# Kernel optimization log

Hardware: AMD Instinct MI355X
Metric: run time of the kernel (lower is better)

The kernel has to match this reference:

```python
import jax, jax.numpy as jnp
import numpy as np
import math

D = 512; H = 8; NL = 6; VOCAB = 256; NC = 10; L = 1024; B = 4
DK = D // H
SCALE = math.sqrt(DK)
EMB_SCALE = math.sqrt(D)
EPS = 1e-5


def _pos_encoding(seq_len, d_model):
    pos = jnp.arange(seq_len, dtype=jnp.float32)[:, None]
    div = jnp.exp(-jnp.arange(0, d_model, 2, dtype=jnp.float32) / d_model * math.log(10000.0))
    pe = jnp.zeros((seq_len, d_model), dtype=jnp.float32)
    pe = pe.at[:, 0::2].set(jnp.sin(pos * div))
    pe = pe.at[:, 1::2].set(jnp.cos(pos * div))
    return pe


def _layer_norm(x, g, b):
    m = jnp.mean(x, axis=-1, keepdims=True)
    v = jnp.mean(jnp.square(x - m), axis=-1, keepdims=True)
    return (x - m) * jax.lax.rsqrt(v + EPS) * g + b


def setup_inputs() -> dict:
    key = jax.random.key(0)
    ks = jax.random.split(key, 18)
    s = 0.02  # keep activations in a sane range so softmax is not saturated
    return {
        "tokens": jax.random.randint(ks[0], (B, L), 0, VOCAB, dtype=jnp.int32),
        "emb_table": jax.random.normal(ks[1], (VOCAB, D), jnp.float32) * s,
        "Wq": jax.random.normal(ks[2], (NL, D, D), jnp.float32) * s,
        "bq": jax.random.normal(ks[3], (NL, D), jnp.float32) * s,
        "Wkv": jax.random.normal(ks[4], (NL, 2 * D, D), jnp.float32) * s,
        "bkv": jax.random.normal(ks[5], (NL, 2 * D), jnp.float32) * s,
        "Wo": jax.random.normal(ks[6], (NL, D, D), jnp.float32) * s,
        "bo": jax.random.normal(ks[7], (NL, D), jnp.float32) * s,
        "ln1_g": jnp.ones((NL, D), jnp.float32),
        "ln1_b": jnp.zeros((NL, D), jnp.float32),
        "W1": jax.random.normal(ks[8], (NL, 4 * D, D), jnp.float32) * s,
        "b1": jax.random.normal(ks[9], (NL, 4 * D), jnp.float32) * s,
        "W2": jax.random.normal(ks[10], (NL, D, 4 * D), jnp.float32) * s,
        "b2": jax.random.normal(ks[11], (NL, D), jnp.float32) * s,
        "ln2_g": jnp.ones((NL, D), jnp.float32),
        "ln2_b": jnp.zeros((NL, D), jnp.float32),
        "Wc": jax.random.normal(ks[12], (NC, D), jnp.float32) * s,
        "bc": jax.random.normal(ks[13], (NC,), jnp.float32) * s,
    }


def reference(tokens, emb_table, Wq, bq, Wkv, bkv, Wo, bo, ln1_g, ln1_b,
              W1, b1, W2, b2, ln2_g, ln2_b, Wc, bc):
    seq_len = tokens.shape[1]
    pe = _pos_encoding(seq_len, D)  # [L, D]
    x = emb_table[tokens] * EMB_SCALE + pe[None]  # [B, L, D]  (dropout = identity in eval)

    def block(x, p):
        wq, bq_, wkv, bkv_, wo, bo_, g1, be1, w1, bb1, w2, bb2, g2, be2 = p
        h = _layer_norm(x, g1, be1)
        q = h @ wq.T + bq_                       # [B, L, D]
        kv = h @ wkv.T + bkv_                    # [B, L, 2D]
        k, v = kv[..., :D], kv[..., D:]
        # split heads: [B, H, L, dk]
        q = q.reshape(*q.shape[:2], H, DK).transpose(0, 2, 1, 3)
        k = k.reshape(*k.shape[:2], H, DK).transpose(0, 2, 1, 3)
        v = v.reshape(*v.shape[:2], H, DK).transpose(0, 2, 1, 3)
        score = jnp.einsum('bhqd,bhkd->bhqk', q, k) / SCALE  # [B, H, L, L]
        attn = jax.nn.softmax(score, axis=-1)
        av = jnp.einsum('bhqk,bhkd->bhqd', attn, v)
        av = av.transpose(0, 2, 1, 3).reshape(*x.shape)      # merge heads
        x = x + (av @ wo.T + bo_)
        h2 = _layer_norm(x, g2, be2)
        ffn = jax.nn.relu(h2 @ w1.T + bb1) @ w2.T + bb2
        x = x + ffn
        return x, None

    params = (Wq, bq, Wkv, bkv, Wo, bo, ln1_g, ln1_b, W1, b1, W2, b2, ln2_g, ln2_b)
    x, _ = jax.lax.scan(block, x, params)
    return x @ Wc.T + bc  # [B, L, NC]
```

## Files before the change

### kernel.cpp

```cpp
#include <hip/hip_runtime.h>
#include <math.h>

#define D 512
#define HEADS 8
#define NLAYER 6
#define LSEQ 1024
#define BATCH 4
#define DKH 64
#define MTOK (BATCH*LSEQ)
#define EPS 1e-5f
#define EMB_SCALE 22.627416997969522f
#define INV_SCALE 0.125f

typedef __attribute__((ext_vector_type(8))) __bf16 bf16x8;
typedef __attribute__((ext_vector_type(4))) float f32x4;

__device__ __forceinline__ unsigned short f2bf(float x) {
    union { float f; unsigned u; } v; v.f = x;
    unsigned r = (v.u + 0x7FFFu + ((v.u >> 16) & 1u)) >> 16;
    return (unsigned short)r;
}
__device__ __forceinline__ unsigned pack2(float a, float b) {
    return (unsigned)f2bf(a) | ((unsigned)f2bf(b) << 16);
}
__device__ __forceinline__ void gl_lds16(const unsigned short* g, unsigned short* l) {
    __builtin_amdgcn_global_load_lds(
        (const __attribute__((address_space(1))) unsigned*)g,
        (__attribute__((address_space(3))) unsigned*)l, 16, 0, 0);
}
__device__ __forceinline__ void gload16(bf16x8& d, const unsigned short* p) {
    asm volatile("global_load_dwordx4 %0, %1, off" : "=v"(d) : "v"(p));
}

__global__ __launch_bounds__(256) void prep_kernel(
    const int* __restrict__ tokens, const float* __restrict__ emb,
    const float* __restrict__ Wq, const float* __restrict__ Wkv,
    const float* __restrict__ Wo, const float* __restrict__ W1,
    const float* __restrict__ W2, const float* __restrict__ bq,
    const float* __restrict__ bkv, unsigned short* __restrict__ wl,
    float* __restrict__ wbias, float* __restrict__ x)
{
    const int bid = blockIdx.x;
    if (bid < 9216) {
        const int l = bid / 1536;
        const int e = (bid - l * 1536) * 2048 + threadIdx.x * 8;
        const float* src;
        if      (e < 262144)  src = Wq  + (size_t)l * 262144  + e;
        else if (e < 786432)  src = Wkv + (size_t)l * 524288  + (e - 262144);
        else if (e < 1048576) src = Wo  + (size_t)l * 262144  + (e - 786432);
        else if (e < 2097152) src = W1  + (size_t)l * 1048576 + (e - 1048576);
        else                  src = W2  + (size_t)l * 1048576 + (e - 2097152);
        float4 a = *(const float4*)src;
        float4 b = *(const float4*)(src + 4);
        uint4 o;
        o.x = pack2(a.x, a.y); o.y = pack2(a.z, a.w);
        o.z = pack2(b.x, b.y); o.w = pack2(b.z, b.w);
        *(uint4*)(wl + (size_t)l * 3145728 + e) = o;
    } else if (bid == 9216) {
        for (int i = threadIdx.x; i < 9216; i += 256) {
            int l = i / 1536, j = i - l * 1536;
            wbias[i] = (j < 512) ? bq[l * 512 + j] : bkv[l * 1024 + (j - 512)];
        }
    } else {
        int row = (bid - 9217) * 2 + (threadIdx.x >> 7);
        int pos = row & (LSEQ - 1);
        int tok = tokens[row];
        int c = (threadIdx.x & 127) * 4;
        float4 e = *(const float4*)(emb + (size_t)tok * D + c);
        float o[4] = {e.x, e.y, e.z, e.w};
#pragma unroll
        for (int i = 0; i < 4; ++i) {
            int col = c + i;
            int ii = col & ~1;
            float dv = expf(-(float)ii * (9.210340371976184f / (float)D));
            float a = (float)pos * dv;
            float pe = (col & 1) ? cosf(a) : sinf(a);
            o[i] = o[i] * EMB_SCALE + pe;
        }
        float4 r; r.x = o[0]; r.y = o[1]; r.z = o[2]; r.w = o[3];
        *(float4*)(x + (size_t)row * D + c) = r;
    }
}

__global__ __launch_bounds__(256) void ln_kernel(
    const float* __restrict__ x, const float* __restrict__ g,
    const float* __restrict__ b, unsigned short* __restrict__ h)
{
    int lane = threadIdx.x & 63;
    int row = blockIdx.x * 4 + (threadIdx.x >> 6);
    const float* xr = x + (size_t)row * D + lane * 8;
    float4 v0 = *(const float4*)(xr);
    float4 v1 = *(const float4*)(xr + 4);
    float s = v0.x + v0.y + v0.z + v0.w + v1.x + v1.y + v1.z + v1.w;
#pragma unroll
    for (int off = 32; off; off >>= 1) s += __shfl_xor(s, off, 64);
    float m = s * (1.0f / D);
    float d0 = v0.x - m, d1 = v0.y - m, d2 = v0.z - m, d3 = v0.w - m;
    float d4 = v1.x - m, d5 = v1.y - m, d6 = v1.z - m, d7 = v1.w - m;
    float ss = d0*d0 + d1*d1 + d2*d2 + d3*d3 + d4*d4 + d5*d5 + d6*d6 + d7*d7;
#pragma unroll
    for (int off = 32; off; off >>= 1) ss += __shfl_xor(ss, off, 64);
    float inv = rsqrtf(ss * (1.0f / D) + EPS);
    const float* gp = g + lane * 8;
    const float* bp = b + lane * 8;
    float4 g0 = *(const float4*)(gp), g1 = *(const float4*)(gp + 4);
    float4 b0 = *(const float4*)(bp), b1 = *(const float4*)(bp + 4);
    uint4 o;
    o.x = pack2(d0 * inv * g0.x + b0.x, d1 * inv * g0.y + b0.y);
    o.y = pack2(d2 * inv * g0.z + b0.z, d3 * inv * g0.w + b0.w);
    o.z = pack2(d4 * inv * g1.x + b1.x, d5 * inv * g1.y + b1.y);
    o.w = pack2(d6 * inv * g1.z + b1.z, d7 * inv * g1.w + b1.w);
    *(uint4*)(h + (size_t)row * D + lane * 8) = o;
}

template<int OMODE, int BM, int BN, int BK>
__global__ __launch_bounds__(256) void gemm_bf16(
    const unsigned short* __restrict__ A, const unsigned short* __restrict__ W,
    const float* __restrict__ bias, const float* __restrict__ X,
    void* __restrict__ C, void* __restrict__ C2, void* __restrict__ C3,
    int M, int N, int K)
{
    constexpr int WM = BM / 64;
    constexpr int WN = 4 / WM;
    constexpr int NI = BN / (WN * 16);
    constexpr int CPB = BK / 8;
    constexpr int RPP = 2048 / BK;
    __shared__ __align__(16) unsigned short As[2][BM * BK];
    __shared__ __align__(16) unsigned short Bs[2][BN * BK];
    const int tid = threadIdx.x;
    const int wave = tid >> 6, lane = tid & 63;
    const int quad = lane >> 4, l16 = lane & 15;
    const int wm = wave / WN, wn = wave % WN;
    const int bm = blockIdx.y * BM, bn = blockIdx.x * BN;

    const int rS  = tid / CPB;
    const int ch  = tid % CPB;
    const int csw = ((ch ^ (rS & 7)) << 3);
    const unsigned short* Asrc = A + (size_t)(bm + rS) * K + csw;
    const unsigned short* Bsrc = W + (size_t)(bn + rS) * K + csw;

    f32x4 acc[4][NI];
#pragma unroll
    for (int mi = 0; mi < 4; ++mi)
#pragma unroll
        for (int ni = 0; ni < NI; ++ni) acc[mi][ni] = (f32x4){0.f, 0.f, 0.f, 0.f};

    const int nt = K / BK;

#pragma unroll
    for (int i = 0; i < BM / RPP; ++i)
        gl_lds16(Asrc + (size_t)(i * RPP) * K, &As[0][i * 2048 + tid * 8]);
#pragma unroll
    for (int i = 0; i < BN / RPP; ++i)
        gl_lds16(Bsrc + (size_t)(i * RPP) * K, &Bs[0][i * 2048 + tid * 8]);
    __syncthreads();

    for (int t = 0; t < nt; ++t) {
        const int cur = t & 1;
        if (t + 1 < nt) {
            const int k0 = (t + 1) * BK;
#pragma unroll
            for (int i = 0; i < BM / RPP; ++i)
                gl_lds16(Asrc + (size_t)(i * RPP) * K + k0, &As[cur ^ 1][i * 2048 + tid * 8]);
#pragma unroll
            for (int i = 0; i < BN / RPP; ++i)
                gl_lds16(Bsrc + (size_t)(i * RPP) * K + k0, &Bs[cur ^ 1][i * 2048 + tid * 8]);
        }
#pragma unroll
        for (int kc = 0; kc < BK / 32; ++kc) {
            const int gch = (kc << 2) | quad;
            bf16x8 af[4], bfr[NI];
#pragma unroll
            for (int mi = 0; mi < 4; ++mi) {
                const int ra = wm * 64 + mi * 16 + l16;
                af[mi] = *(const bf16x8*)&As[cur][ra * BK + ((gch ^ (ra & 7)) << 3)];
            }
#pragma unroll
            for (int ni = 0; ni < NI; ++ni) {
                const int rb = wn * (BN / WN) + ni * 16 + l16;
                bfr[ni] = *(const bf16x8*)&Bs[cur][rb * BK + ((gch ^ (rb & 7)) << 3)];
            }
#pragma unroll
            for (int mi = 0; mi < 4; ++mi)
#pragma unroll
                for (int ni = 0; ni < NI; ++ni)
                    acc[mi][ni] = __builtin_amdgcn_mfma_f32_16x16x32_bf16(
                        af[mi], bfr[ni], acc[mi][ni], 0, 0, 0);
        }
        __syncthreads();
    }

    const int er = bm + wm * 64;
    const int ec = bn + wn * (BN / WN);

    if (OMODE == 0) {
        float* Cf = (float*)C;
#pragma unroll
        for (int ni = 0; ni < NI; ++ni) {
            int c = ec + ni * 16 + l16;
            float bv = bias[c];
#pragma unroll
            for (int mi = 0; mi < 4; ++mi)
#pragma unroll
                for (int r = 0; r < 4; ++r) {
                    int m = er + mi * 16 + quad * 4 + r;
                    Cf[(size_t)m * N + c] = acc[mi][ni][r] + bv + X[(size_t)m * N + c];
                }
        }
    } else if (OMODE == 1) {
        unsigned short* Cb = (unsigned short*)C;
#pragma unroll
        for (int ni = 0; ni < NI; ++ni) {
            int c = ec + ni * 16 + l16;
            float bv = bias[c];
#pragma unroll
            for (int mi = 0; mi < 4; ++mi)
#pragma unroll
                for (int r = 0; r < 4; ++r) {
                    int m = er + mi * 16 + quad * 4 + r;
                    Cb[(size_t)m * N + c] = f2bf(fmaxf(acc[mi][ni][r] + bv, 0.f));
                }
        }
    } else {
        if (bn < 512) {
            unsigned short* Qp = (unsigned short*)C;
#pragma unroll
            for (int ni = 0; ni < NI; ++ni) {
                int c = ec + ni * 16 + l16;
                float bv = bias[c];
                int hh = c >> 6, dd = c & 63;
                size_t cbase = (size_t)(dd >> 5) * 512 + (size_t)((dd >> 3) & 3) * 128 + (dd & 7);
#pragma unroll
                for (int mi = 0; mi < 4; ++mi)
#pragma unroll
                    for (int r = 0; r < 4; ++r) {
                        int m = er + mi * 16 + quad * 4 + r;
                        int b = m >> 10, t = m & 1023;
                        Qp[(size_t)(b * 8 + hh) * 65536 + (size_t)(t >> 4) * 1024
                           + cbase + (size_t)(t & 15) * 8] =
                            f2bf((acc[mi][ni][r] + bv) * INV_SCALE);
                    }
            }
        } else if (bn < 1024) {
            unsigned short* Kp = (unsigned short*)C2;
#pragma unroll
            for (int ni = 0; ni < NI; ++ni) {
                int c = ec + ni * 16 + l16;
                float bv = bias[c];
                int c2 = c - 512;
                int hh = c2 >> 6, dd = c2 & 63;
                size_t cbase = (size_t)(dd >> 5) * 512 + (size_t)((dd >> 3) & 3) * 128 + (dd & 7);
#pragma unroll
                for (int mi = 0; mi < 4; ++mi)
#pragma unroll
                    for (int r = 0; r < 4; ++r) {
                        int m = er + mi * 16 + quad * 4 + r;
                        int b = m >> 10, t = m & 1023;
                        Kp[(size_t)(b * 8 + hh) * 65536 + (size_t)(t >> 4) * 1024
                           + cbase + (size_t)(t & 15) * 8] =
                            f2bf(acc[mi][ni][r] + bv);
                    }
            }
        } else {
            unsigned short* Vp = (unsigned short*)C3;
#pragma unroll
            for (int ni = 0; ni < NI; ++ni) {
                int c = ec + ni * 16 + l16;
                float bv = bias[c];
                int c2 = c - 1024;
                int hh = c2 >> 6, dd = c2 & 63;
                size_t dbase = (size_t)(dd >> 4) * 16384 + (size_t)(dd & 15) * 8;
#pragma unroll
                for (int mi = 0; mi < 4; ++mi) {
                    int t0 = er + mi * 16 + quad * 4;
                    int b = t0 >> 10, tt = t0 & 1023;
                    ushort4 o;
                    o.x = f2bf(acc[mi][ni][0] + bv);
                    o.y = f2bf(acc[mi][ni][1] + bv);
                    o.z = f2bf(acc[mi][ni][2] + bv);
                    o.w = f2bf(acc[mi][ni][3] + bv);
                    *(ushort4*)(Vp + (size_t)(b * 8 + hh) * 65536 + dbase
                                + (size_t)(tt >> 5) * 512
                                + (size_t)((tt >> 3) & 3) * 128 + (tt & 7)) = o;
                }
            }
        }
    }
}

__global__ __launch_bounds__(256, 1) void attn_mfma(
    const unsigned short* __restrict__ Qb, const unsigned short* __restrict__ Kb,
    const unsigned short* __restrict__ Vt, unsigned short* __restrict__ av)
{
    __shared__ float Ol[4][32][68];
    __shared__ float Ls[4][32];
    const int tid = threadIdx.x;
    const int wave = tid >> 6, lane = tid & 63;
    const int quad = lane >> 4, l16 = lane & 15;
    const int bh = blockIdx.x & 31;
    const int b = bh >> 3, h = bh & 7;
    const int q0 = (blockIdx.x >> 5) * 32;

    const unsigned short* qp = Qb + (size_t)bh * 65536 + (size_t)(q0 >> 4) * 1024 + lane * 8;
    const unsigned short* kbase = Kb + (size_t)bh * 65536 + lane * 8;
    const unsigned short* vbase = Vt + (size_t)bh * 65536 + lane * 8;

    const int sA  = ((((2 * quad) & 3) << 4) + l16) << 2;
    const int sB2 = ((((2 * quad + 1) & 3) << 4) + l16) << 2;

    f32x4 o[2][4];
#pragma unroll
    for (int qs = 0; qs < 2; ++qs)
#pragma unroll
        for (int nf = 0; nf < 4; ++nf) o[qs][nf] = (f32x4){0.f, 0.f, 0.f, 0.f};
    float lp[2] = {0.f, 0.f};

    const int j0 = wave * 256;

    bf16x8 qf[2][2];
    gload16(qf[0][0], qp);
    gload16(qf[0][1], qp + 512);
    gload16(qf[1][0], qp + 1024);
    gload16(qf[1][1], qp + 1536);

    bf16x8 kc[2][8], vf[2][8];
#pragma unroll
    for (int nf = 0; nf < 4; ++nf) {
        gload16(kc[0][2 * nf],     kbase + (size_t)j0 * 64 + nf * 1024);
        gload16(kc[0][2 * nf + 1], kbase + (size_t)j0 * 64 + nf * 1024 + 512);
        gload16(vf[0][2 * nf],     vbase + (size_t)j0 * 16 + nf * 16384);
        gload16(vf[0][2 * nf + 1], vbase + (size_t)j0 * 16 + nf * 16384 + 512);
    }

#pragma unroll
    for (int it = 0; it < 4; ++it) {
        const int cur = it & 1, nxt = cur ^ 1;
        if (it < 3) {
            const int jn = j0 + (it + 1) * 64;
#pragma unroll
            for (int nf = 0; nf < 4; ++nf) {
                gload16(kc[nxt][2 * nf],     kbase + (size_t)jn * 64 + nf * 1024);
                gload16(kc[nxt][2 * nf + 1], kbase + (size_t)jn * 64 + nf * 1024 + 512);
                gload16(vf[nxt][2 * nf],     vbase + (size_t)jn * 16 + nf * 16384);
                gload16(vf[nxt][2 * nf + 1], vbase + (size_t)jn * 16 + nf * 16384 + 512);
            }
        }
        if (it < 3) asm volatile("s_waitcnt vmcnt(16)" ::: "memory");
        else        asm volatile("s_waitcnt vmcnt(0)"  ::: "memory");
        __builtin_amdgcn_sched_barrier(0);
        unsigned pk01[2][4], pk23[2][4];
#pragma unroll
        for (int nf = 0; nf < 4; ++nf)
#pragma unroll
            for (int qs = 0; qs < 2; ++qs) {
                f32x4 z = {0.f, 0.f, 0.f, 0.f};
                z = __builtin_amdgcn_mfma_f32_16x16x32_bf16(kc[cur][2 * nf], qf[qs][0], z, 0, 0, 0);
                z = __builtin_amdgcn_mfma_f32_16x16x32_bf16(kc[cur][2 * nf + 1], qf[qs][1], z, 0, 0, 0);
                float p0 = __expf(z[0]);
                float p1 = __expf(z[1]);
                float p2 = __expf(z[2]);
                float p3 = __expf(z[3]);
                lp[qs] += (p0 + p1) + (p2 + p3);
                pk01[qs][nf] = pack2(p0, p1);
                pk23[qs][nf] = pack2(p2, p3);
            }
#pragma unroll
        for (int qs = 0; qs < 2; ++qs) {
            union PU { unsigned d[4]; bf16x8 v; } f0, f1;
            unsigned a0, a1;
            a0 = (unsigned)__builtin_amdgcn_ds_bpermute(sA,  (int)pk01[qs][0]);
            a1 = (unsigned)__builtin_amdgcn_ds_bpermute(sA,  (int)pk01[qs][1]);
            f0.d[0] = (quad < 2) ? a0 : a1;
            a0 = (unsigned)__builtin_amdgcn_ds_bpermute(sA,  (int)pk23[qs][0]);
            a1 = (unsigned)__builtin_amdgcn_ds_bpermute(sA,  (int)pk23[qs][1]);
            f0.d[1] = (quad < 2) ? a0 : a1;
            a0 = (unsigned)__builtin_amdgcn_ds_bpermute(sB2, (int)pk01[qs][0]);
            a1 = (unsigned)__builtin_amdgcn_ds_bpermute(sB2, (int)pk01[qs][1]);
            f0.d[2] = (quad < 2) ? a0 : a1;
            a0 = (unsigned)__builtin_amdgcn_ds_bpermute(sB2, (int)pk23[qs][0]);
            a1 = (unsigned)__builtin_amdgcn_ds_bpermute(sB2, (int)pk23[qs][1]);
            f0.d[3] = (quad < 2) ? a0 : a1;
            a0 = (unsigned)__builtin_amdgcn_ds_bpermute(sA,  (int)pk01[qs][2]);
            a1 = (unsigned)__builtin_amdgcn_ds_bpermute(sA,  (int)pk01[qs][3]);
            f1.d[0] = (quad < 2) ? a0 : a1;
            a0 = (unsigned)__builtin_amdgcn_ds_bpermute(sA,  (int)pk23[qs][2]);
            a1 = (unsigned)__builtin_amdgcn_ds_bpermute(sA,  (int)pk23[qs][3]);
            f1.d[1] = (quad < 2) ? a0 : a1;
            a0 = (unsigned)__builtin_amdgcn_ds_bpermute(sB2, (int)pk01[qs][2]);
            a1 = (unsigned)__builtin_amdgcn_ds_bpermute(sB2, (int)pk01[qs][3]);
            f1.d[2] = (quad < 2) ? a0 : a1;
            a0 = (unsigned)__builtin_amdgcn_ds_bpermute(sB2, (int)pk23[qs][2]);
            a1 = (unsigned)__builtin_amdgcn_ds_bpermute(sB2, (int)pk23[qs][3]);
            f1.d[3] = (quad < 2) ? a0 : a1;
#pragma unroll
            for (int nf = 0; nf < 4; ++nf) {
                o[qs][nf] = __builtin_amdgcn_mfma_f32_16x16x32_bf16(f0.v, vf[cur][2 * nf], o[qs][nf], 0, 0, 0);
                o[qs][nf] = __builtin_amdgcn_mfma_f32_16x16x32_bf16(f1.v, vf[cur][2 * nf + 1], o[qs][nf], 0, 0, 0);
            }
        }
    }
#pragma unroll
    for (int qs = 0; qs < 2; ++qs)
#pragma unroll
        for (int nf = 0; nf < 4; ++nf)
#pragma unroll
            for (int r = 0; r < 4; ++r)
                Ol[wave][qs * 16 + quad * 4 + r][nf * 16 + l16] = o[qs][nf][r];
#pragma unroll
    for (int qs = 0; qs < 2; ++qs) {
        float ts = lp[qs];
        ts += __shfl_xor(ts, 16, 64);
        ts += __shfl_xor(ts, 32, 64);
        if (quad == 0) Ls[wave][qs * 16 + l16] = ts;
    }
    __syncthreads();
#pragma unroll
    for (int half = 0; half < 2; ++half)
#pragma unroll
        for (int r = 0; r < 4; ++r) {
            int qq = half * 16 + quad * 4 + r;
            float denom = Ls[0][qq] + Ls[1][qq] + Ls[2][qq] + Ls[3][qq];
            float v = Ol[0][qq][wave * 16 + l16] + Ol[1][qq][wave * 16 + l16]
                    + Ol[2][qq][wave * 16 + l16] + Ol[3][qq][wave * 16 + l16];
            int q = q0 + qq;
            av[((size_t)(b * 1024 + q)) * D + h * 64 + wave * 16 + l16] =
                f2bf(v / denom);
        }
}

__global__ __launch_bounds__(256) void cls_kernel(
    const float* __restrict__ x, const float* __restrict__ Wc,
    const float* __restrict__ bc, float* __restrict__ out)
{
    int lane = threadIdx.x & 63;
    int row = blockIdx.x * 4 + (threadIdx.x >> 6);
    const float* xr = x + (size_t)row * D + lane * 8;
    float4 v0 = *(const float4*)xr;
    float4 v1 = *(const float4*)(xr + 4);
    float acc[10];
#pragma unroll
    for (int c = 0; c < 10; ++c) {
        const float* wr = Wc + c * D + lane * 8;
        float4 w0 = *(const float4*)wr;
        float4 w1 = *(const float4*)(wr + 4);
        acc[c] = v0.x*w0.x + v0.y*w0.y + v0.z*w0.z + v0.w*w0.w
               + v1.x*w1.x + v1.y*w1.y + v1.z*w1.z + v1.w*w1.w;
    }
#pragma unroll
    for (int c = 0; c < 10; ++c)
#pragma unroll
        for (int off = 32; off; off >>= 1) acc[c] += __shfl_xor(acc[c], off, 64);
    if (lane == 0) {
#pragma unroll
        for (int c = 0; c < 10; ++c) out[(size_t)row * 10 + c] = acc[c] + bc[c];
    }
}

extern "C" void kernel_launch(void* const* d_in, const int* in_sizes, int n_in,
                              void* d_out, int out_size, void* d_ws, size_t ws_size,
                              hipStream_t stream)
{
    const int*   tokens = (const int*)  d_in[0];
    const float* emb    = (const float*)d_in[1];
    const float* Wq     = (const float*)d_in[2];
    const float* bq     = (const float*)d_in[3];
    const float* Wkv    = (const float*)d_in[4];
    const float* bkv    = (const float*)d_in[5];
    const float* Wo     = (const float*)d_in[6];
    const float* bo     = (const float*)d_in[7];
    const float* ln1g   = (const float*)d_in[8];
    const float* ln1b   = (const float*)d_in[9];
    const float* W1     = (const float*)d_in[10];
    const float* b1     = (const float*)d_in[11];
    const float* W2     = (const float*)d_in[12];
    const float* b2     = (const float*)d_in[13];
    const float* ln2g   = (const float*)d_in[14];
    const float* ln2b   = (const float*)d_in[15];
    const float* Wc     = (const float*)d_in[16];
    const float* bc     = (const float*)d_in[17];
    float* out = (float*)d_out;

    float* x  = (float*)d_ws;
    unsigned short* hb  = (unsigned short*)(x + (size_t)MTOK * D);
    unsigned short* Qb  = hb  + (size_t)MTOK * D;
    unsigned short* Kb  = Qb  + (size_t)32 * 1024 * 64;
    unsigned short* Vt  = Kb  + (size_t)32 * 1024 * 64;
    unsigned short* avb = Vt  + (size_t)32 * 1024 * 64;
    unsigned short* f1b = Qb;
    unsigned short* wl  = avb + (size_t)32 * 1024 * 64;
    float* wbias = (float*)(wl + (size_t)6 * 3145728);

    const size_t oWo = 786432, oW1 = 1048576, oW2 = 2097152, LW = 3145728;

    prep_kernel<<<11265, 256, 0, stream>>>(
        tokens, emb, Wq, Wkv, Wo, W1, W2, bq, bkv, wl, wbias, x);

    for (int l = 0; l < NLAYER; ++l) {
        const unsigned short* wll = wl + (size_t)l * LW;
        ln_kernel<<<MTOK / 4, 256, 0, stream>>>(x, ln1g + l * D, ln1b + l * D, hb);
        gemm_bf16<2,128,64,64><<<dim3(24, 32), 256, 0, stream>>>(
            hb, wll, wbias + l * 1536, nullptr, Qb, Kb, Vt, MTOK, 1536, 512);
        attn_mfma<<<1024, 256, 0, stream>>>(Qb, Kb, Vt, avb);
        gemm_bf16<0,64,64,128><<<dim3(8, 64), 256, 0, stream>>>(
            avb, wll + oWo, bo + l * D, x, x, nullptr, nullptr, MTOK, D, D);
        ln_kernel<<<MTOK / 4, 256, 0, stream>>>(x, ln2g + l * D, ln2b + l * D, hb);
        gemm_bf16<1,128,128,64><<<dim3(16, 32), 256, 0, stream>>>(
            hb, wll + oW1, b1 + l * 4 * D, nullptr, f1b, nullptr, nullptr, MTOK, 4 * D, D);
        gemm_bf16<0,64,64,128><<<dim3(8, 64), 256, 0, stream>>>(
            f1b, wll + oW2, b2 + l * D, x, x, nullptr, nullptr, MTOK, D, 4 * D);
    }

    cls_kernel<<<MTOK / 4, 256, 0, stream>>>(x, Wc, bc, out);
}
```

Before: 683.6 us.

## Fold LayerNorm into GEMM epilogues using row stats and gamma-scaled weights

Removes the two per-layer LayerNorm kernels. Gamma is folded into the bf16 weights, and per-output vectors W·gamma and W·beta plus the bias are precomputed in prep. Residual GEMMs now also write a bf16 copy of x and accumulate per-row sum and sum-of-squares with atomics. Consumer GEMMs read raw bf16 x and apply mean and rstd in the epilogue. This trades kernel launches and LN memory passes for atomics and extra epilogue work, and adds precision risk: the E[x²]−mean² variance can cancel, and the GEMM now runs on un-centered bf16 x.

```diff
diff --git a/kernel.cpp b/kernel.cpp
--- a/kernel.cpp
+++ b/kernel.cpp
@@ -34,16 +34,21 @@
 
 __global__ __launch_bounds__(256) void prep_kernel(
     const int* __restrict__ tokens, const float* __restrict__ emb,
-    const float* __restrict__ Wq, const float* __restrict__ Wkv,
+    const float* __restrict__ Wq, const float* __restrict__ bq,
+    const float* __restrict__ Wkv, const float* __restrict__ bkv,
     const float* __restrict__ Wo, const float* __restrict__ W1,
-    const float* __restrict__ W2, const float* __restrict__ bq,
-    const float* __restrict__ bkv, unsigned short* __restrict__ wl,
-    float* __restrict__ wbias, float* __restrict__ x)
+    const float* __restrict__ b1, const float* __restrict__ W2,
+    const float* __restrict__ ln1g, const float* __restrict__ ln1b,
+    const float* __restrict__ ln2g, const float* __restrict__ ln2b,
+    unsigned short* __restrict__ wl, float* __restrict__ vecg,
+    float* __restrict__ vecb, float* __restrict__ stats,
+    float* __restrict__ x, unsigned short* __restrict__ xb)
 {
     const int bid = blockIdx.x;
+    const int tid = threadIdx.x;
     if (bid < 9216) {
         const int l = bid / 1536;
-        const int e = (bid - l * 1536) * 2048 + threadIdx.x * 8;
+        const int e = (bid - l * 1536) * 2048 + tid * 8;
         const float* src;
         if      (e < 262144)  src = Wq  + (size_t)l * 262144  + e;
         else if (e < 786432)  src = Wkv + (size_t)l * 524288  + (e - 262144);
@@ -52,65 +57,88 @@
         else                  src = W2  + (size_t)l * 1048576 + (e - 2097152);
         float4 a = *(const float4*)src;
         float4 b = *(const float4*)(src + 4);
+        const float* gp = nullptr;
+        if (e < 786432)                          gp = ln1g + l * 512;
+        else if (e >= 1048576 && e < 2097152)    gp = ln2g + l * 512;
+        if (gp) {
+            int cb = e & 511;
+            a.x *= gp[cb];     a.y *= gp[cb + 1]; a.z *= gp[cb + 2]; a.w *= gp[cb + 3];
+            b.x *= gp[cb + 4]; b.y *= gp[cb + 5]; b.z *= gp[cb + 6]; b.w *= gp[cb + 7];
+        }
         uint4 o;
         o.x = pack2(a.x, a.y); o.y = pack2(a.z, a.w);
         o.z = pack2(b.x, b.y); o.w = pack2(b.z, b.w);
         *(uint4*)(wl + (size_t)l * 3145728 + e) = o;
-    } else if (bid == 9216) {
-        for (int i = threadIdx.x; i < 9216; i += 256) {
-            int l = i / 1536, j = i - l * 1536;
-            wbias[i] = (j < 512) ? bq[l * 512 + j] : bkv[l * 1024 + (j - 512)];
-        }
+    } else if (bid < 14592) {
+        const int lane = tid & 63, wave = tid >> 6;
+        const int out = (bid - 9216) * 4 + wave;
+        const float *wrow, *g, *bl;
+        float bias;
+        if (out < 9216) {
+            int l = out / 1536, n = out - l * 1536;
+            wrow = (n < 512) ? Wq + (size_t)l * 262144 + (size_t)n * 512
+                             : Wkv + (size_t)l * 524288 + (size_t)(n - 512) * 512;
+            g = ln1g + l * 512; bl = ln1b + l * 512;
+            bias = (n < 512) ? bq[l * 512 + n] : bkv[l * 1024 + (n - 512)];
+        } else {
+            int o2 = out - 9216;
+            int l = o2 / 2048, n = o2 - l * 2048;
+            wrow = W1 + (size_t)l * 1048576 + (size_t)n * 512;
+            g = ln2g + l * 512; bl = ln2b + l * 512;
+            bias = b1[l * 2048 + n];
+        }
+        const float* wp = wrow + lane * 8;
+        float4 w0 = *(const float4*)wp,       w1 = *(const float4*)(wp + 4);
+        float4 g0 = *(const float4*)(g + lane * 8),  g1 = *(const float4*)(g + lane * 8 + 4);
+        float4 c0 = *(const float4*)(bl + lane * 8), c1 = *(const float4*)(bl + lane * 8 + 4);
+        float sg = w0.x*g0.x + w0.y*g0.y + w0.z*g0.z + w0.w*g0.w
+                 + w1.x*g1.x + w1.y*g1.y + w1.z*g1.z + w1.w*g1.w;
+        float sb = w0.x*c0.x + w0.y*c0.y + w0.z*c0.z + w0.w*c0.w
+                 + w1.x*c1.x + w1.y*c1.y + w1.z*c1.z + w1.w*c1.w;
+#pragma unroll
+        for (int off = 32; off; off >>= 1) {
+            sg += __shfl_xor(sg, off, 64);
+            sb += __shfl_xor(sb, off, 64);
+        }
+        if (lane == 0) { vecg[out] = sg; vecb[out] = sb + bias; }
+    } else if (bid < 14688) {
+        int i = (bid - 14592) * 1024 + tid * 4;
+        *(float4*)&stats[8192 + i] = (float4){0.f, 0.f, 0.f, 0.f};
     } else {
-        int row = (bid - 9217) * 2 + (threadIdx.x >> 7);
+        int row = (bid - 14688) * 4 + (tid >> 6);
+        int lane = tid & 63;
         int pos = row & (LSEQ - 1);
         int tok = tokens[row];
-        int c = (threadIdx.x & 127) * 4;
-        float4 e = *(const float4*)(emb + (size_t)tok * D + c);
-        float o[4] = {e.x, e.y, e.z, e.w};
-#pragma unroll
-        for (int i = 0; i < 4; ++i) {
-            int col = c + i;
-            int ii = col & ~1;
+        int c = lane * 8;
+        const float* ep = emb + (size_t)tok * D + c;
+        float4 e0 = *(const float4*)ep;
+        float4 e1 = *(const float4*)(ep + 4);
+        float v[8] = {e0.x, e0.y, e0.z, e0.w, e1.x, e1.y, e1.z, e1.w};
+        float s = 0.f, ss = 0.f;
+#pragma unroll
+        for (int i = 0; i < 8; ++i) {
+            int col = c + i, ii = col & ~1;
             float dv = expf(-(float)ii * (9.210340371976184f / (float)D));
             float a = (float)pos * dv;
             float pe = (col & 1) ? cosf(a) : sinf(a);
-            o[i] = o[i] * EMB_SCALE + pe;
-        }
-        float4 r; r.x = o[0]; r.y = o[1]; r.z = o[2]; r.w = o[3];
-        *(float4*)(x + (size_t)row * D + c) = r;
-    }
-}
-
-__global__ __launch_bounds__(256) void ln_kernel(
-    const float* __restrict__ x, const float* __restrict__ g,
-    const float* __restrict__ b, unsigned short* __restrict__ h)
-{
-    int lane = threadIdx.x & 63;
-    int row = blockIdx.x * 4 + (threadIdx.x >> 6);
-    const float* xr = x + (size_t)row * D + lane * 8;
-    float4 v0 = *(const float4*)(xr);
-    float4 v1 = *(const float4*)(xr + 4);
-    float s = v0.x + v0.y + v0.z + v0.w + v1.x + v1.y + v1.z + v1.w;
-#pragma unroll
-    for (int off = 32; off; off >>= 1) s += __shfl_xor(s, off, 64);
-    float m = s * (1.0f / D);
-    float d0 = v0.x - m, d1 = v0.y - m, d2 = v0.z - m, d3 = v0.w - m;
-    float d4 = v1.x - m, d5 = v1.y - m, d6 = v1.z - m, d7 = v1.w - m;
-    float ss = d0*d0 + d1*d1 + d2*d2 + d3*d3 + d4*d4 + d5*d5 + d6*d6 + d7*d7;
-#pragma unroll
-    for (int off = 32; off; off >>= 1) ss += __shfl_xor(ss, off, 64);
-    float inv = rsqrtf(ss * (1.0f / D) + EPS);
-    const float* gp = g + lane * 8;
-    const float* bp = b + lane * 8;
-    float4 g0 = *(const float4*)(gp), g1 = *(const float4*)(gp + 4);
-    float4 b0 = *(const float4*)(bp), b1 = *(const float4*)(bp + 4);
-    uint4 o;
-    o.x = pack2(d0 * inv * g0.x + b0.x, d1 * inv * g0.y + b0.y);
-    o.y = pack2(d2 * inv * g0.z + b0.z, d3 * inv * g0.w + b0.w);
-    o.z = pack2(d4 * inv * g1.x + b1.x, d5 * inv * g1.y + b1.y);
-    o.w = pack2(d6 * inv * g1.z + b1.z, d7 * inv * g1.w + b1.w);
-    *(uint4*)(h + (size_t)row * D + lane * 8) = o;
+            v[i] = v[i] * EMB_SCALE + pe;
+            s += v[i]; ss += v[i] * v[i];
+        }
+        float4 r0; r0.x = v[0]; r0.y = v[1]; r0.z = v[2]; r0.w = v[3];
+        float4 r1; r1.x = v[4]; r1.y = v[5]; r1.z = v[6]; r1.w = v[7];
+        *(float4*)(x + (size_t)row * D + c) = r0;
+        *(float4*)(x + (size_t)row * D + c + 4) = r1;
+        uint4 ob;
+        ob.x = pack2(v[0], v[1]); ob.y = pack2(v[2], v[3]);
+        ob.z = pack2(v[4], v[5]); ob.w = pack2(v[6], v[7]);
+        *(uint4*)(xb + (size_t)row * D + c) = ob;
+#pragma unroll
+        for (int off = 1; off < 64; off <<= 1) {
+            s  += __shfl_xor(s,  off, 64);
+            ss += __shfl_xor(ss, off, 64);
+        }
+        if (lane == 0) { stats[row * 2] = s; stats[row * 2 + 1] = ss; }
+    }
 }
 
 template<int OMODE, int BM, int BN, int BK>
@@ -118,6 +146,9 @@
     const unsigned short* __restrict__ A, const unsigned short* __restrict__ W,
     const float* __restrict__ bias, const float* __restrict__ X,
     void* __restrict__ C, void* __restrict__ C2, void* __restrict__ C3,
+    const float* __restrict__ lstats, const float* __restrict__ vg,
+    const float* __restrict__ vb, float* __restrict__ statsOut,
+    unsigned short* __restrict__ xbOut,
     int M, int N, int K)
 {
     constexpr int WM = BM / 64;
@@ -196,92 +227,119 @@
     if (OMODE == 0) {
         float* Cf = (float*)C;
 #pragma unroll
-        for (int ni = 0; ni < NI; ++ni) {
-            int c = ec + ni * 16 + l16;
-            float bv = bias[c];
-#pragma unroll
-            for (int mi = 0; mi < 4; ++mi)
-#pragma unroll
-                for (int r = 0; r < 4; ++r) {
-                    int m = er + mi * 16 + quad * 4 + r;
-                    Cf[(size_t)m * N + c] = acc[mi][ni][r] + bv + X[(size_t)m * N + c];
+        for (int mi = 0; mi < 4; ++mi)
+#pragma unroll
+            for (int r = 0; r < 4; ++r) {
+                int m = er + mi * 16 + quad * 4 + r;
+                float s = 0.f, sq = 0.f;
+#pragma unroll
+                for (int ni = 0; ni < NI; ++ni) {
+                    int c = ec + ni * 16 + l16;
+                    float val = acc[mi][ni][r] + bias[c] + X[(size_t)m * N + c];
+                    Cf[(size_t)m * N + c] = val;
+                    xbOut[(size_t)m * N + c] = f2bf(val);
+                    s += val; sq += val * val;
                 }
-        }
-    } else if (OMODE == 1) {
-        unsigned short* Cb = (unsigned short*)C;
-#pragma unroll
-        for (int ni = 0; ni < NI; ++ni) {
-            int c = ec + ni * 16 + l16;
-            float bv = bias[c];
-#pragma unroll
-            for (int mi = 0; mi < 4; ++mi)
-#pragma unroll
-                for (int r = 0; r < 4; ++r) {
-                    int m = er + mi * 16 + quad * 4 + r;
-                    Cb[(size_t)m * N + c] = f2bf(fmaxf(acc[mi][ni][r] + bv, 0.f));
+#pragma unroll
+                for (int off = 1; off < 16; off <<= 1) {
+                    s  += __shfl_xor(s,  off, 64);
+                    sq += __shfl_xor(sq, off, 64);
                 }
-        }
+                if (l16 == 0) {
+                    atomicAdd(&statsOut[(size_t)m * 2],     s);
+                    atomicAdd(&statsOut[(size_t)m * 2 + 1], sq);
+                }
+            }
     } else {
-        if (bn < 512) {
-            unsigned short* Qp = (unsigned short*)C;
+        float mvv[4][4], ivv[4][4];
+#pragma unroll
+        for (int mi = 0; mi < 4; ++mi)
+#pragma unroll
+            for (int r = 0; r < 4; ++r) {
+                int m = er + mi * 16 + quad * 4 + r;
+                float sm = lstats[(size_t)m * 2];
+                float sq = lstats[(size_t)m * 2 + 1];
+                float mn = sm * (1.0f / D);
+                mvv[mi][r] = mn;
+                ivv[mi][r] = rsqrtf(sq * (1.0f / D) - mn * mn + EPS);
+            }
+        if (OMODE == 1) {
+            unsigned short* Cb = (unsigned short*)C;
 #pragma unroll
             for (int ni = 0; ni < NI; ++ni) {
                 int c = ec + ni * 16 + l16;
-                float bv = bias[c];
-                int hh = c >> 6, dd = c & 63;
-                size_t cbase = (size_t)(dd >> 5) * 512 + (size_t)((dd >> 3) & 3) * 128 + (dd & 7);
+                float vgc = vg[c], vbc = vb[c];
 #pragma unroll
                 for (int mi = 0; mi < 4; ++mi)
 #pragma unroll
                     for (int r = 0; r < 4; ++r) {
                         int m = er + mi * 16 + quad * 4 + r;
-                        int b = m >> 10, t = m & 1023;
-                        Qp[(size_t)(b * 8 + hh) * 65536 + (size_t)(t >> 4) * 1024
-                           + cbase + (size_t)(t & 15) * 8] =
-                            f2bf((acc[mi][ni][r] + bv) * INV_SCALE);
+                        float val = ivv[mi][r] * (acc[mi][ni][r] - mvv[mi][r] * vgc) + vbc;
+                        Cb[(size_t)m * N + c] = f2bf(fmaxf(val, 0.f));
                     }
             }
-        } else if (bn < 1024) {
-            unsigned short* Kp = (unsigned short*)C2;
-#pragma unroll
-            for (int ni = 0; ni < NI; ++ni) {
-                int c = ec + ni * 16 + l16;
-                float bv = bias[c];
-                int c2 = c - 512;
-                int hh = c2 >> 6, dd = c2 & 63;
-                size_t cbase = (size_t)(dd >> 5) * 512 + (size_t)((dd >> 3) & 3) * 128 + (dd & 7);
-#pragma unroll
-                for (int mi = 0; mi < 4; ++mi)
-#pragma unroll
-                    for (int r = 0; r < 4; ++r) {
-                        int m = er + mi * 16 + quad * 4 + r;
-                        int b = m >> 10, t = m & 1023;
-                        Kp[(size_t)(b * 8 + hh) * 65536 + (size_t)(t >> 4) * 1024
-                           + cbase + (size_t)(t & 15) * 8] =
-                            f2bf(acc[mi][ni][r] + bv);
+        } else {
+            if (bn < 512) {
+                unsigned short* Qp = (unsigned short*)C;
+#pragma unroll
+                for (int ni = 0; ni < NI; ++ni) {
+                    int c = ec + ni * 16 + l16;
+                    float vgc = vg[c], vbc = vb[c];
+                    int hh = c >> 6, dd = c & 63;
+                    size_t cbase = (size_t)(dd >> 5) * 512 + (size_t)((dd >> 3) & 3) * 128 + (dd & 7);
+#pragma unroll
+                    for (int mi = 0; mi < 4; ++mi)
+#pragma unroll
+                        for (int r = 0; r < 4; ++r) {
+                            int m = er + mi * 16 + quad * 4 + r;
+                            int b = m >> 10, t = m & 1023;
+                            float val = ivv[mi][r] * (acc[mi][ni][r] - mvv[mi][r] * vgc) + vbc;
+                            Qp[(size_t)(b * 8 + hh) * 65536 + (size_t)(t >> 4) * 1024
+                               + cbase + (size_t)(t & 15) * 8] = f2bf(val * INV_SCALE);
+                        }
+                }
+            } else if (bn < 1024) {
+                unsigned short* Kp = (unsigned short*)C2;
+#pragma unroll
+                for (int ni = 0; ni < NI; ++ni) {
+                    int c = ec + ni * 16 + l16;
+                    float vgc = vg[c], vbc = vb[c];
+                    int c2 = c - 512;
+                    int hh = c2 >> 6, dd = c2 & 63;
+                    size_t cbase = (size_t)(dd >> 5) * 512 + (size_t)((dd >> 3) & 3) * 128 + (dd & 7);
+#pragma unroll
+                    for (int mi = 0; mi < 4; ++mi)
+#pragma unroll
+                        for (int r = 0; r < 4; ++r) {
+                            int m = er + mi * 16 + quad * 4 + r;
+                            int b = m >> 10, t = m & 1023;
+                            float val = ivv[mi][r] * (acc[mi][ni][r] - mvv[mi][r] * vgc) + vbc;
+                            Kp[(size_t)(b * 8 + hh) * 65536 + (size_t)(t >> 4) * 1024
+                               + cbase + (size_t)(t & 15) * 8] = f2bf(val);
+                        }
+                }
+            } else {
+                unsigned short* Vp = (unsigned short*)C3;
+#pragma unroll
+                for (int ni = 0; ni < NI; ++ni) {
+                    int c = ec + ni * 16 + l16;
+                    float vgc = vg[c], vbc = vb[c];
+                    int c2 = c - 1024;
+                    int hh = c2 >> 6, dd = c2 & 63;
+                    size_t dbase = (size_t)(dd >> 4) * 16384 + (size_t)(dd & 15) * 8;
+#pragma unroll
+                    for (int mi = 0; mi < 4; ++mi) {
+                        int t0 = er + mi * 16 + quad * 4;
+                        int b = t0 >> 10, tt = t0 & 1023;
+                        ushort4 o;
+                        o.x = f2bf(ivv[mi][0] * (acc[mi][ni][0] - mvv[mi][0] * vgc) + vbc);
+                        o.y = f2bf(ivv[mi][1] * (acc[mi][ni][1] - mvv[mi][1] * vgc) + vbc);
+                        o.z = f2bf(ivv[mi][2] * (acc[mi][ni][2] - mvv[mi][2] * vgc) + vbc);
+                        o.w = f2bf(ivv[mi][3] * (acc[mi][ni][3] - mvv[mi][3] * vgc) + vbc);
+                        *(ushort4*)(Vp + (size_t)(b * 8 + hh) * 65536 + dbase
+                                    + (size_t)(tt >> 5) * 512
+                                    + (size_t)((tt >> 3) & 3) * 128 + (tt & 7)) = o;
                     }
-            }
-        } else {
-            unsigned short* Vp = (unsigned short*)C3;
-#pragma unroll
-            for (int ni = 0; ni < NI; ++ni) {
-                int c = ec + ni * 16 + l16;
-                float bv = bias[c];
-                int c2 = c - 1024;
-                int hh = c2 >> 6, dd = c2 & 63;
-                size_t dbase = (size_t)(dd >> 4) * 16384 + (size_t)(dd & 15) * 8;
-#pragma unroll
-                for (int mi = 0; mi < 4; ++mi) {
-                    int t0 = er + mi * 16 + quad * 4;
-                    int b = t0 >> 10, tt = t0 & 1023;
-                    ushort4 o;
-                    o.x = f2bf(acc[mi][ni][0] + bv);
-                    o.y = f2bf(acc[mi][ni][1] + bv);
-                    o.z = f2bf(acc[mi][ni][2] + bv);
-                    o.w = f2bf(acc[mi][ni][3] + bv);
-                    *(ushort4*)(Vp + (size_t)(b * 8 + hh) * 65536 + dbase
-                                + (size_t)(tt >> 5) * 512
-                                + (size_t)((tt >> 3) & 3) * 128 + (tt & 7)) = o;
                 }
             }
         }
@@ -481,33 +539,43 @@
     float* out = (float*)d_out;
 
     float* x  = (float*)d_ws;
-    unsigned short* hb  = (unsigned short*)(x + (size_t)MTOK * D);
-    unsigned short* Qb  = hb  + (size_t)MTOK * D;
+    unsigned short* xb  = (unsigned short*)(x + (size_t)MTOK * D);
+    unsigned short* Qb  = xb  + (size_t)MTOK * D;
     unsigned short* Kb  = Qb  + (size_t)32 * 1024 * 64;
     unsigned short* Vt  = Kb  + (size_t)32 * 1024 * 64;
     unsigned short* avb = Vt  + (size_t)32 * 1024 * 64;
     unsigned short* f1b = Qb;
     unsigned short* wl  = avb + (size_t)32 * 1024 * 64;
-    float* wbias = (float*)(wl + (size_t)6 * 3145728);
+    float* vecg  = (float*)(wl + (size_t)6 * 3145728);
+    float* vecb  = vecg + 21504;
+    float* stats = vecb + 21504;
 
     const size_t oWo = 786432, oW1 = 1048576, oW2 = 2097152, LW = 3145728;
 
-    prep_kernel<<<11265, 256, 0, stream>>>(
-        tokens, emb, Wq, Wkv, Wo, W1, W2, bq, bkv, wl, wbias, x);
+    prep_kernel<<<15712, 256, 0, stream>>>(
+        tokens, emb, Wq, bq, Wkv, bkv, Wo, W1, b1, W2,
+        ln1g, ln1b, ln2g, ln2b, wl, vecg, vecb, stats, x, xb);
 
     for (int l = 0; l < NLAYER; ++l) {
         const unsigned short* wll = wl + (size_t)l * LW;
-        ln_kernel<<<MTOK / 4, 256, 0, stream>>>(x, ln1g + l * D, ln1b + l * D, hb);
+        float* sl1  = stats + (size_t)l * 8192;
+        float* sl1n = stats + (size_t)(l + 1) * 8192;
+        float* sl2  = stats + (size_t)(7 + l) * 8192;
         gemm_bf16<2,128,64,64><<<dim3(24, 32), 256, 0, stream>>>(
-            hb, wll, wbias + l * 1536, nullptr, Qb, Kb, Vt, MTOK, 1536, 512);
+            xb, wll, nullptr, nullptr, Qb, Kb, Vt,
+            sl1, vecg + l * 1536, vecb + l * 1536, nullptr, nullptr,
+            MTOK, 1536, 512);
         attn_mfma<<<1024, 256, 0, stream>>>(Qb, Kb, Vt, avb);
         gemm_bf16<0,64,64,128><<<dim3(8, 64), 256, 0, stream>>>(
-            avb, wll + oWo, bo + l * D, x, x, nullptr, nullptr, MTOK, D, D);
-        ln_kernel<<<MTOK / 4, 256, 0, stream>>>(x, ln2g + l * D, ln2b + l * D, hb);
+            avb, wll + oWo, bo + l * D, x, x, nullptr, nullptr,
+            nullptr, nullptr, nullptr, sl2, xb, MTOK, D, D);
         gemm_bf16<1,128,128,64><<<dim3(16, 32), 256, 0, stream>>>(
-            hb, wll + oW1, b1 + l * 4 * D, nullptr, f1b, nullptr, nullptr, MTOK, 4 * D, D);
+            xb, wll + oW1, nullptr, nullptr, f1b, nullptr, nullptr,
+            sl2, vecg + 9216 + l * 2048, vecb + 9216 + l * 2048, nullptr, nullptr,
+            MTOK, 4 * D, D);
         gemm_bf16<0,64,64,128><<<dim3(8, 64), 256, 0, stream>>>(
-            f1b, wll + oW2, b2 + l * D, x, x, nullptr, nullptr, MTOK, D, 4 * D);
+            f1b, wll + oW2, b2 + l * D, x, x, nullptr, nullptr,
+            nullptr, nullptr, nullptr, sl1n, xb, MTOK, D, 4 * D);
     }
 
     cls_kernel<<<MTOK / 4, 256, 0, stream>>>(x, Wc, bc, out);
```

Result: slower. 797.5 us (+16.7%).
